# Optimization experiments

Measured on AMD Instinct MI355X. Metric: run time of the kernel, lower is better.

## Reference

```python
import math
import jax, jax.numpy as jnp
import numpy as np

N_EMBED = 1024
N_HEAD = 16
B, T = 2, 2048


def _gelu_tanh(x):
    # GPT-2 tanh-approx GELU
    c = math.sqrt(2.0 / math.pi)
    return 0.5 * x * (1.0 + jnp.tanh(c * (x + 0.044715 * x * x * x)))


def _layer_norm(x, w, b, eps=1e-5):
    mu = jnp.mean(x, axis=-1, keepdims=True)
    var = jnp.var(x, axis=-1, keepdims=True)
    return (x - mu) * jax.lax.rsqrt(var + eps) * w + b


def setup_inputs() -> dict:
    key = jax.random.key(0)
    ks = jax.random.split(key, 8)
    s = lambda fan_in: 1.0 / math.sqrt(fan_in)
    return {
        "x": jax.random.normal(ks[0], (B, T, N_EMBED), jnp.float32),
        "ln1_w": jnp.ones((N_EMBED,), jnp.float32),
        "ln1_b": jnp.zeros((N_EMBED,), jnp.float32),
        "W_attn": jax.random.normal(ks[1], (N_EMBED, 3 * N_EMBED), jnp.float32) * s(N_EMBED),
        "b_attn": jnp.zeros((3 * N_EMBED,), jnp.float32),
        "W_o": jax.random.normal(ks[2], (N_EMBED, N_EMBED), jnp.float32) * s(N_EMBED),
        "b_o": jnp.zeros((N_EMBED,), jnp.float32),
        "ln2_w": jnp.ones((N_EMBED,), jnp.float32),
        "ln2_b": jnp.zeros((N_EMBED,), jnp.float32),
        "W_fc": jax.random.normal(ks[3], (N_EMBED, 4 * N_EMBED), jnp.float32) * s(N_EMBED),
        "b_fc": jnp.zeros((4 * N_EMBED,), jnp.float32),
        "W_proj": jax.random.normal(ks[4], (4 * N_EMBED, N_EMBED), jnp.float32) * s(4 * N_EMBED),
        "b_proj": jnp.zeros((N_EMBED,), jnp.float32),
    }


def reference(x, ln1_w, ln1_b, W_attn, b_attn, W_o, b_o,
              ln2_w, ln2_b, W_fc, b_fc, W_proj, b_proj):
    Bx, Tx, C = x.shape
    H = N_HEAD
    Dh = C // H

    # --- attention ---
    h = _layer_norm(x, ln1_w, ln1_b)
    qkv = h @ W_attn + b_attn                       # [B,T,3C]
    q, k, v = jnp.split(qkv, 3, axis=-1)
    q = q.reshape(Bx, Tx, H, Dh).transpose(0, 2, 1, 3)   # [B,H,T,Dh]
    k = k.reshape(Bx, Tx, H, Dh).transpose(0, 2, 1, 3)
    v = v.reshape(Bx, Tx, H, Dh).transpose(0, 2, 1, 3)

    attn = jnp.einsum("bhqd,bhkd->bhqk", q, k) * (1.0 / math.sqrt(Dh))
    causal = jnp.tril(jnp.ones((Tx, Tx), dtype=bool))
    attn = jnp.where(causal[None, None], attn, -jnp.inf)
    attn = jax.nn.softmax(attn, axis=-1)
    y = jnp.einsum("bhqk,bhkd->bhqd", attn, v)      # [B,H,T,Dh]
    y = y.transpose(0, 2, 1, 3).reshape(Bx, Tx, C)
    y = y @ W_o + b_o
    x = x + y

    # --- MLP ---
    h = _layer_norm(x, ln2_w, ln2_b)
    h = _gelu_tanh(h @ W_fc + b_fc)
    h = h @ W_proj + b_proj
    return x + h
```

## Files before the change

kernel.cpp:

```cpp
#include <hip/hip_runtime.h>
#include <math.h>

constexpr int TDIM = 2048;
constexpr int BDIM = 2;
constexpr int CDIM = 1024;
constexpr int HEADS = 16;
constexpr int DH = 64;
constexpr int MDIM = BDIM * TDIM;

typedef short bf16x8 __attribute__((ext_vector_type(8)));
typedef float f32x4 __attribute__((ext_vector_type(4)));
typedef float f32x16 __attribute__((ext_vector_type(16)));

__device__ __forceinline__ float b2f(unsigned short u) {
    union { float f; unsigned int i; } v; v.i = ((unsigned int)u) << 16; return v.f;
}
__device__ __forceinline__ unsigned short f2b(float f) {
    union { float f; unsigned int i; } v; v.f = f;
    unsigned int r = (v.i + 0x7FFFu + ((v.i >> 16) & 1u)) >> 16;
    return (unsigned short)r;
}
__device__ __forceinline__ unsigned int cvtpk(float lo, float hi) {
    unsigned int r;
    asm("v_cvt_pk_bf16_f32 %0, %1, %2" : "=v"(r) : "v"(lo), "v"(hi));
    return r;
}
__device__ __forceinline__ float gelu_f(float x) {
    float z = -2.3022077f * (x + 0.044715f * x * x * x);
    return x / (1.0f + exp2f(z));
}
__device__ __forceinline__ void async_copy16(const void* g, void* l) {
    __builtin_amdgcn_global_load_lds(
        (const __attribute__((address_space(1))) unsigned int*)g,
        (__attribute__((address_space(3))) unsigned int*)l, 16, 0, 0);
}

#define PBAR do { asm volatile("" ::: "memory"); __builtin_amdgcn_s_barrier(); \
                  asm volatile("" ::: "memory"); } while (0)
#define LGKM0 asm volatile("s_waitcnt lgkmcnt(0)" ::: "memory")

__global__ __launch_bounds__(256) void transpose_cast(
    const float* __restrict__ W, unsigned short* __restrict__ Wt, int K, int N) {
    __shared__ float tile[32][33];
    int n0 = blockIdx.x * 32, k0 = blockIdx.y * 32;
    int tx = threadIdx.x & 31, ty = threadIdx.x >> 5;
#pragma unroll
    for (int i = 0; i < 32; i += 8)
        tile[ty + i][tx] = W[(size_t)(k0 + ty + i) * N + n0 + tx];
    __syncthreads();
#pragma unroll
    for (int i = 0; i < 32; i += 8)
        Wt[(size_t)(n0 + ty + i) * K + k0 + tx] = f2b(tile[tx][ty + i]);
}

__global__ __launch_bounds__(256) void ln_kernel(
    const float* __restrict__ x, const float* __restrict__ w,
    const float* __restrict__ b, unsigned short* __restrict__ out) {
    int row = blockIdx.x;
    int tid = threadIdx.x;
    const float* xr = x + (size_t)row * CDIM;
    float4 v = *(const float4*)(xr + tid * 4);
    float s  = v.x + v.y + v.z + v.w;
    float ss = v.x * v.x + v.y * v.y + v.z * v.z + v.w * v.w;
#pragma unroll
    for (int off = 32; off >= 1; off >>= 1) {
        s  += __shfl_xor(s, off);
        ss += __shfl_xor(ss, off);
    }
    __shared__ float rs[4], rss[4];
    int wave = tid >> 6;
    if ((tid & 63) == 0) { rs[wave] = s; rss[wave] = ss; }
    __syncthreads();
    s  = rs[0] + rs[1] + rs[2] + rs[3];
    ss = rss[0] + rss[1] + rss[2] + rss[3];
    float mean = s * (1.0f / CDIM);
    float var  = ss * (1.0f / CDIM) - mean * mean;
    float rstd = rsqrtf(var + 1e-5f);
    float4 wv = *(const float4*)(w + tid * 4);
    float4 bv = *(const float4*)(b + tid * 4);
    ushort4 o;
    o.x = f2b((v.x - mean) * rstd * wv.x + bv.x);
    o.y = f2b((v.y - mean) * rstd * wv.y + bv.y);
    o.z = f2b((v.z - mean) * rstd * wv.z + bv.z);
    o.w = f2b((v.w - mean) * rstd * wv.w + bv.w);
    *(ushort4*)(out + (size_t)row * CDIM + tid * 4) = o;
}

template <int MODE>
__global__ __launch_bounds__(512, 2) void gemm256(
    const unsigned short* __restrict__ A, const unsigned short* __restrict__ Wt,
    const float* __restrict__ bias, void* __restrict__ Cout, int M, int N, int K) {
    __shared__ __align__(16) short As[2][256 * 64];
    __shared__ __align__(16) short Bs[2][256 * 64];
    const int tid = threadIdx.x;
    const int lane = tid & 63, w = tid >> 6;
    const int wm = w >> 2, wn = w & 3;
    const int h = lane >> 4, r15 = lane & 15;
    const int sr = lane >> 3;
    const int sc = 8 * ((lane & 7) ^ sr);

    const int nwg = gridDim.x * gridDim.y;
    const int bid = blockIdx.y * gridDim.x + blockIdx.x;
    const int nbid = (bid & 7) * (nwg >> 3) + (bid >> 3);
    const int bx = nbid % gridDim.x;
    const int by = nbid / gridDim.x;
    const int row0 = by * 256, col0 = bx * 256;

    const unsigned short* gA = A  + (size_t)(row0 + w * 8 + sr) * K + sc;
    const unsigned short* gB = Wt + (size_t)(col0 + w * 8 + sr) * K + sc;

    f32x4 acc[8][4] = {};
    bf16x8 aA[4][2], bB[4][2];

    auto stA = [&](int kt, int hh) {
        short* dst = &As[kt & 1][(hh * 128 + w * 8) * 64];
        const unsigned short* src = gA + (size_t)(hh * 128) * K + (size_t)kt * 64;
        async_copy16(src, dst);
        async_copy16(src + (size_t)64 * K, dst + 64 * 64);
    };
    auto stB = [&](int kt, int hh) {
        short* dst = &Bs[kt & 1][(hh * 128 + w * 8) * 64];
        const unsigned short* src = gB + (size_t)(hh * 128) * K + (size_t)kt * 64;
        async_copy16(src, dst);
        async_copy16(src + (size_t)64 * K, dst + 64 * 64);
    };
    auto rdA = [&](const short* S, int rh) {
#pragma unroll
        for (int ii = 0; ii < 4; ++ii)
#pragma unroll
            for (int ks = 0; ks < 2; ++ks) {
                int ra = wm * 128 + rh * 64 + ii * 16 + r15;
                int off = ra * 128 + ((ks * 64 + h * 16) ^ ((ra & 7) << 4));
                aA[ii][ks] = *(const bf16x8*)((const char*)S + off);
            }
    };
    auto rdB = [&](const short* S, int J0) {
#pragma unroll
        for (int dj = 0; dj < 2; ++dj)
#pragma unroll
            for (int ks = 0; ks < 2; ++ks) {
                int rb = wn * 64 + (J0 + dj) * 16 + r15;
                int off = rb * 128 + ((ks * 64 + h * 16) ^ ((rb & 7) << 4));
                bB[J0 + dj][ks] = *(const bf16x8*)((const char*)S + off);
            }
    };
    auto mm = [&](int rh, int ch) {
        __builtin_amdgcn_s_setprio(1);
#pragma unroll
        for (int ii = 0; ii < 4; ++ii)
#pragma unroll
            for (int jj = 0; jj < 2; ++jj)
#pragma unroll
                for (int ks = 0; ks < 2; ++ks)
                    acc[rh * 4 + ii][ch * 2 + jj] = __builtin_amdgcn_mfma_f32_16x16x32_bf16(
                        aA[ii][ks], bB[ch * 2 + jj][ks], acc[rh * 4 + ii][ch * 2 + jj], 0, 0, 0);
        __builtin_amdgcn_s_setprio(0);
    };

    const int niter = K >> 7;

    stA(0, 0); stB(0, 0); stB(0, 1); stA(0, 1);
    stA(1, 0); stB(1, 0); stB(1, 1);
    asm volatile("s_waitcnt vmcnt(6)" ::: "memory");
    PBAR;

    for (int t = 0; t < niter; ++t) {
        const bool st = (t + 1 < niter);
        const int t2 = 2 * t + 2, t3 = 2 * t + 3;
        rdA(As[0], 0); rdB(Bs[0], 0);
        stA(2 * t + 1, 1);
        PBAR; LGKM0; mm(0, 0); PBAR;
        rdB(Bs[0], 2);
        PBAR; LGKM0; mm(0, 1); PBAR;
        rdA(As[0], 1);
        if (st) stB(t2, 0);
        PBAR; LGKM0; mm(1, 0); PBAR;
        if (st) {
            stB(t2, 1);
            stA(t2, 0);
            asm volatile("s_waitcnt vmcnt(6)" ::: "memory");
        } else {
            asm volatile("s_waitcnt vmcnt(0)" ::: "memory");
        }
        PBAR; LGKM0; mm(1, 1); PBAR;
        rdA(As[1], 0); rdB(Bs[1], 0);
        if (st) stA(t2, 1);
        PBAR; LGKM0; mm(0, 0); PBAR;
        rdB(Bs[1], 2);
        PBAR; LGKM0; mm(0, 1); PBAR;
        rdA(As[1], 1);
        if (st) stB(t3, 0);
        PBAR; LGKM0; mm(1, 0); PBAR;
        if (st) {
            stB(t3, 1);
            stA(t3, 0);
            asm volatile("s_waitcnt vmcnt(6)" ::: "memory");
        } else {
            asm volatile("s_waitcnt vmcnt(0)" ::: "memory");
        }
        PBAR; LGKM0; mm(1, 1); PBAR;
    }

#pragma unroll
    for (int I = 0; I < 8; ++I) {
#pragma unroll
        for (int J = 0; J < 4; ++J) {
            int cc = col0 + wn * 64 + J * 16 + r15;
            float bv = bias[cc];
#pragma unroll
            for (int q = 0; q < 4; ++q) {
                int rr = row0 + wm * 128 + I * 16 + h * 4 + q;
                float v = acc[I][J][q] + bv;
                if (MODE == 2) v = gelu_f(v);
                ((unsigned short*)Cout)[(size_t)rr * N + cc] = f2b(v);
            }
        }
    }
}

template <int MODE, int BN, int NBUF>
__global__ __launch_bounds__(256) void gemm_bf16(
    const unsigned short* __restrict__ A, const unsigned short* __restrict__ Wt,
    const float* __restrict__ bias, const float* __restrict__ res,
    void* __restrict__ Cout, int M, int N, int K) {
    constexpr int JF = BN / 32;
    constexpr int INF = 4 + JF;
    __shared__ __align__(16) short As[NBUF][128 * 64];
    __shared__ __align__(16) short Bs[NBUF][BN * 64];
    const int tid = threadIdx.x;
    const int lane = tid & 63, w = tid >> 6;
    const int wr = w >> 1, wc = w & 1;

    const int nwg = gridDim.x * gridDim.y;
    const int bid = blockIdx.y * gridDim.x + blockIdx.x;
    const int nbid = (bid & 7) * (nwg >> 3) + (bid >> 3);
    const int bx = nbid % gridDim.x;
    const int by = nbid / gridDim.x;
    const int row0 = by * 128, col0 = bx * BN;

    const int sr = lane >> 3;
    const int sc = 8 * ((lane & 7) ^ sr);
    const unsigned short* gA = A  + (size_t)(row0 + w * 8 + sr) * K + sc;
    const unsigned short* gB = Wt + (size_t)(col0 + w * 8 + sr) * K + sc;

    f32x4 acc[4][JF] = {};
    const int h = lane >> 4;
    const int r15 = lane & 15;
    const int nt = K >> 6;

#pragma unroll
    for (int pt = 0; pt < NBUF - 1; ++pt) {
        const int kp = pt << 6;
#pragma unroll
        for (int i = 0; i < 4; ++i)
            async_copy16(gA + (size_t)i * 32 * K + kp, &As[pt][(w * 8 + i * 32) * 64]);
#pragma unroll
        for (int i = 0; i < JF; ++i)
            async_copy16(gB + (size_t)i * 32 * K + kp, &Bs[pt][(w * 8 + i * 32) * 64]);
    }

    for (int t = 0; t < nt; ++t) {
        const int cur = t % NBUF;
        const int tp = t + NBUF - 1;
        if (tp < nt) {
            const int bufp = tp % NBUF;
            const int kp = tp << 6;
#pragma unroll
            for (int i = 0; i < 4; ++i)
                async_copy16(gA + (size_t)i * 32 * K + kp, &As[bufp][(w * 8 + i * 32) * 64]);
#pragma unroll
            for (int i = 0; i < JF; ++i)
                async_copy16(gB + (size_t)i * 32 * K + kp, &Bs[bufp][(w * 8 + i * 32) * 64]);
            asm volatile("s_waitcnt vmcnt(%0)" :: "n"((NBUF - 1) * INF) : "memory");
        } else {
            asm volatile("s_waitcnt vmcnt(0)" ::: "memory");
        }
        __builtin_amdgcn_s_barrier();
        asm volatile("" ::: "memory");

#pragma unroll
        for (int ks = 0; ks < 2; ++ks) {
            bf16x8 af[4], bfr[JF];
#pragma unroll
            for (int i = 0; i < 4; ++i) {
                int ra = wr * 64 + i * 16 + r15;
                int offa = ra * 128 + ((ks * 64 + h * 16) ^ ((ra & 7) << 4));
                af[i] = *(const bf16x8*)((const char*)As[cur] + offa);
            }
#pragma unroll
            for (int j = 0; j < JF; ++j) {
                int rb = wc * (BN / 2) + j * 16 + r15;
                int offb = rb * 128 + ((ks * 64 + h * 16) ^ ((rb & 7) << 4));
                bfr[j] = *(const bf16x8*)((const char*)Bs[cur] + offb);
            }
#pragma unroll
            for (int i = 0; i < 4; ++i)
#pragma unroll
                for (int j = 0; j < JF; ++j)
                    acc[i][j] = __builtin_amdgcn_mfma_f32_16x16x32_bf16(
                        af[i], bfr[j], acc[i][j], 0, 0, 0);
        }
        asm volatile("" ::: "memory");
        __builtin_amdgcn_s_barrier();
    }

#pragma unroll
    for (int i = 0; i < 4; ++i) {
#pragma unroll
        for (int j = 0; j < JF; ++j) {
            int c = col0 + wc * (BN / 2) + j * 16 + r15;
            float bv = bias[c];
#pragma unroll
            for (int q = 0; q < 4; ++q) {
                int rr = row0 + wr * 64 + i * 16 + h * 4 + q;
                float v = acc[i][j][q] + bv;
                if (MODE == 2) v = gelu_f(v);
                if (MODE == 1) v += res[(size_t)rr * N + c];
                if (MODE == 1) ((float*)Cout)[(size_t)rr * N + c] = v;
                else ((unsigned short*)Cout)[(size_t)rr * N + c] = f2b(v);
            }
        }
    }
}

__global__ __launch_bounds__(512, 4) void attn_mfma(
    const unsigned short* __restrict__ qkv, unsigned short* __restrict__ y) {
    const int bh = blockIdx.x;
    const int b = bh >> 4, hh = bh & 15;
    const int by = blockIdx.y;
    const int qy = (by < 8) ? (15 - by) : (by - 8);
    const int q0 = qy * 128;
    const int tid = threadIdx.x;
    const int lane = tid & 63, w = tid >> 6;
    const int p = w & 3, half = w >> 2;
    const int hi = lane >> 5, q31 = lane & 31;

    const float SC  = 0.1803368801111244f;
    const float THR = 44.0f;

    __shared__ __align__(16) char smem[36864];
    float (*Os)[68] = (float (*)[68])smem;
    float* mlm = (float*)(smem + 34816);
    float* mll = (float*)(smem + 34816 + 1024);

    const size_t base = (size_t)b * TDIM * (3 * CDIM);
    const unsigned short* qb = qkv + base + hh * DH;
    const unsigned short* kb = qkv + base + CDIM + hh * DH;
    const unsigned short* vb = qkv + base + 2 * CDIM + hh * DH;

    const int gq = q0 + p * 32 + q31;
    const int qmin_w = q0 + p * 32;
    const int qmax_w = qmin_w + 31;

    bf16x8 qf[4];
#pragma unroll
    for (int ks = 0; ks < 4; ++ks)
        qf[ks] = *(const bf16x8*)(qb + (size_t)gq * (3 * CDIM) + ks * 16 + hi * 8);

    const int sr = lane >> 3;
    const int scK = 8 * ((lane & 7) ^ sr);
    const int rV = tid >> 3;
    const int dblk = (tid & 7) * 8;

    f32x16 oacc[2] = {};
    float m = -1e30f, l = 0.f;
    bf16x8 vreg;

    const int NT = 2 * qy + 2;

    {
        short* Ks0 = (short*)smem;
        int rowbase = w * 8;
        async_copy16(kb + (size_t)(rowbase + sr) * (3 * CDIM) + scK, Ks0 + rowbase * 64);
        vreg = *(const bf16x8*)(vb + (size_t)rV * (3 * CDIM) + dblk);
        char* Vt0 = smem + 16384;
#pragma unroll
        for (int j = 0; j < 8; ++j) {
            int d = dblk + j;
            int swz = ((d ^ (d >> 3)) & 7) << 4;
            *(short*)(Vt0 + d * 128 + ((2 * rV) ^ swz)) = vreg[j];
        }
    }
    __syncthreads();

    for (int kt = 0; kt < NT; ++kt) {
        const int c = kt & 1;
        const char* Ksc = smem + c * 8192;
        const char* Vtc = smem + 16384 + c * 8192;
        const bool pre = (kt + 1 < NT);

        if (pre) {
            const int kv1 = (kt + 1) * 64;
            short* Ksn = (short*)(smem + (c ^ 1) * 8192);
            int rowbase = w * 8;
            async_copy16(kb + (size_t)(kv1 + rowbase + sr) * (3 * CDIM) + scK,
                         Ksn + rowbase * 64);
            vreg = *(const bf16x8*)(vb + (size_t)(kv1 + rV) * (3 * CDIM) + dblk);
        }

        const int kvs = kt * 64 + half * 32;
        if (kvs <= qmax_w) {
            f32x16 sacc = {};
            __builtin_amdgcn_s_setprio(1);
#pragma unroll
            for (int ks = 0; ks < 4; ++ks) {
                int row = half * 32 + q31;
                int off = row * 128 + ((32 * ks + 16 * hi) ^ ((row & 7) << 4));
                bf16x8 kf = *(const bf16x8*)(Ksc + off);
                sacc = __builtin_amdgcn_mfma_f32_32x32x16_bf16(kf, qf[ks], sacc, 0, 0, 0);
            }
            __builtin_amdgcn_s_setprio(0);

            float p_[16];
            if (kvs + 31 > qmin_w) {
#pragma unroll
                for (int r = 0; r < 16; ++r) {
                    int kvg = kvs + (r & 3) + 8 * (r >> 2) + 4 * hi;
                    p_[r] = (kvg > gq) ? -1e30f : sacc[r];
                }
            } else {
#pragma unroll
                for (int r = 0; r < 16; ++r) p_[r] = sacc[r];
            }

            float t8[8];
#pragma unroll
            for (int r = 0; r < 8; ++r) t8[r] = fmaxf(p_[r], p_[r + 8]);
#pragma unroll
            for (int r = 0; r < 4; ++r) t8[r] = fmaxf(t8[r], t8[r + 4]);
            float pm = fmaxf(fmaxf(t8[0], t8[1]), fmaxf(t8[2], t8[3]));
            pm = fmaxf(pm, __shfl_xor(pm, 32));

            if (!__all(pm <= m + THR)) {
                float mnew = fmaxf(m, pm);
                float sf = exp2f((m - mnew) * SC);
                m = mnew;
                l *= sf;
                oacc[0] *= sf;
                oacc[1] *= sf;
            }
            float mc = m * SC;
#pragma unroll
            for (int r = 0; r < 16; ++r) p_[r] = exp2f(fmaf(p_[r], SC, -mc));
#pragma unroll
            for (int r = 0; r < 8; ++r) t8[r] = p_[r] + p_[r + 8];
#pragma unroll
            for (int r = 0; r < 4; ++r) t8[r] = t8[r] + t8[r + 4];
            float rsum = (t8[0] + t8[1]) + (t8[2] + t8[3]);
            rsum += __shfl_xor(rsum, 32);
            l += rsum;

            bf16x8 pa[2];
#pragma unroll
            for (int k2 = 0; k2 < 2; ++k2) {
                unsigned int A0 = cvtpk(p_[8 * k2 + 0], p_[8 * k2 + 1]);
                unsigned int A1 = cvtpk(p_[8 * k2 + 2], p_[8 * k2 + 3]);
                unsigned int B0 = cvtpk(p_[8 * k2 + 4], p_[8 * k2 + 5]);
                unsigned int B1 = cvtpk(p_[8 * k2 + 6], p_[8 * k2 + 7]);
                unsigned int sA0 = __shfl_xor((int)A0, 32);
                unsigned int sA1 = __shfl_xor((int)A1, 32);
                unsigned int sB0 = __shfl_xor((int)B0, 32);
                unsigned int sB1 = __shfl_xor((int)B1, 32);
                union { int i[4]; bf16x8 h; } u;
                u.i[0] = hi ? (int)sB0 : (int)A0;
                u.i[1] = hi ? (int)sB1 : (int)A1;
                u.i[2] = hi ? (int)B0 : (int)sA0;
                u.i[3] = hi ? (int)B1 : (int)sA1;
                pa[k2] = u.h;
            }

            __builtin_amdgcn_s_setprio(1);
#pragma unroll
            for (int j2 = 0; j2 < 2; ++j2) {
                int row = 32 * j2 + q31;
                int swz = ((row ^ (row >> 3)) & 7) << 4;
#pragma unroll
                for (int k2 = 0; k2 < 2; ++k2) {
                    int off = row * 128 + ((64 * half + 32 * k2 + 16 * hi) ^ swz);
                    bf16x8 vf = *(const bf16x8*)(Vtc + off);
                    oacc[j2] = __builtin_amdgcn_mfma_f32_32x32x16_bf16(vf, pa[k2], oacc[j2], 0, 0, 0);
                }
            }
            __builtin_amdgcn_s_setprio(0);
        }

        if (pre) {
            char* Vtn = smem + 16384 + (c ^ 1) * 8192;
#pragma unroll
            for (int j = 0; j < 8; ++j) {
                int d = dblk + j;
                int swz = ((d ^ (d >> 3)) & 7) << 4;
                *(short*)(Vtn + d * 128 + ((2 * rV) ^ swz)) = vreg[j];
            }
        }
        __syncthreads();
    }

    mlm[(half * 4 + p) * 32 + q31] = m;
    mll[(half * 4 + p) * 32 + q31] = l;
    __syncthreads();
    float mo = mlm[((half ^ 1) * 4 + p) * 32 + q31];
    float lo = mll[((half ^ 1) * 4 + p) * 32 + q31];
    float M  = fmaxf(m, mo);
    float sf  = exp2f((m - M) * SC);
    float sfo = exp2f((mo - M) * SC);
    float invl = 1.0f / (l * sf + lo * sfo);

    if (half == 1) {
#pragma unroll
        for (int j2 = 0; j2 < 2; ++j2)
#pragma unroll
            for (int g = 0; g < 4; ++g) {
                float4 v4 = make_float4(oacc[j2][4 * g + 0] * sf, oacc[j2][4 * g + 1] * sf,
                                        oacc[j2][4 * g + 2] * sf, oacc[j2][4 * g + 3] * sf);
                *(float4*)&Os[p * 32 + q31][32 * j2 + 8 * g + 4 * hi] = v4;
            }
    }
    __syncthreads();
    if (half == 0) {
#pragma unroll
        for (int j2 = 0; j2 < 2; ++j2)
#pragma unroll
            for (int g = 0; g < 4; ++g) {
                float4 t = *(const float4*)&Os[p * 32 + q31][32 * j2 + 8 * g + 4 * hi];
                float4 v4;
                v4.x = (oacc[j2][4 * g + 0] * sf + t.x) * invl;
                v4.y = (oacc[j2][4 * g + 1] * sf + t.y) * invl;
                v4.z = (oacc[j2][4 * g + 2] * sf + t.z) * invl;
                v4.w = (oacc[j2][4 * g + 3] * sf + t.w) * invl;
                *(float4*)&Os[p * 32 + q31][32 * j2 + 8 * g + 4 * hi] = v4;
            }
    }
    __syncthreads();

    const int r0 = tid >> 4;
    const int c4 = (tid & 15) * 4;
#pragma unroll
    for (int pass = 0; pass < 4; ++pass) {
        int row = pass * 32 + r0;
        float4 v = *(const float4*)&Os[row][c4];
        ushort4 o;
        o.x = f2b(v.x); o.y = f2b(v.y); o.z = f2b(v.z); o.w = f2b(v.w);
        *(ushort4*)(y + (size_t)(b * TDIM + q0 + row) * CDIM + hh * DH + c4) = o;
    }
}

extern "C" void kernel_launch(void* const* d_in, const int* in_sizes, int n_in,
                              void* d_out, int out_size, void* d_ws, size_t ws_size,
                              hipStream_t stream) {
    const float* x      = (const float*)d_in[0];
    const float* ln1_w  = (const float*)d_in[1];
    const float* ln1_b  = (const float*)d_in[2];
    const float* W_attn = (const float*)d_in[3];
    const float* b_attn = (const float*)d_in[4];
    const float* W_o    = (const float*)d_in[5];
    const float* b_o    = (const float*)d_in[6];
    const float* ln2_w  = (const float*)d_in[7];
    const float* ln2_b  = (const float*)d_in[8];
    const float* W_fc   = (const float*)d_in[9];
    const float* b_fc   = (const float*)d_in[10];
    const float* W_proj = (const float*)d_in[11];
    const float* b_proj = (const float*)d_in[12];
    float* out = (float*)d_out;

    char* ws = (char*)d_ws;
    const size_t MB = 1024 * 1024;
    unsigned short* h_bf    = (unsigned short*)(ws);
    unsigned short* big     = (unsigned short*)(ws + 8 * MB);
    unsigned short* Wt_attn = (unsigned short*)(ws + 40 * MB);
    unsigned short* Wt_o    = (unsigned short*)(ws + 46 * MB);
    unsigned short* Wt_fc   = (unsigned short*)(ws + 48 * MB);
    unsigned short* Wt_proj = (unsigned short*)(ws + 56 * MB);
    float* x1 = out;

    hipLaunchKernelGGL(transpose_cast, dim3(96, 32),  dim3(256), 0, stream, W_attn, Wt_attn, CDIM, 3 * CDIM);
    hipLaunchKernelGGL(transpose_cast, dim3(32, 32),  dim3(256), 0, stream, W_o,    Wt_o,    CDIM, CDIM);
    hipLaunchKernelGGL(transpose_cast, dim3(128, 32), dim3(256), 0, stream, W_fc,   Wt_fc,   CDIM, 4 * CDIM);
    hipLaunchKernelGGL(transpose_cast, dim3(32, 128), dim3(256), 0, stream, W_proj, Wt_proj, 4 * CDIM, CDIM);

    hipLaunchKernelGGL(ln_kernel, dim3(MDIM), dim3(256), 0, stream, x, ln1_w, ln1_b, h_bf);
    hipLaunchKernelGGL((gemm256<0>), dim3(3 * CDIM / 256, MDIM / 256), dim3(512), 0,
                       stream, h_bf, Wt_attn, b_attn, big, MDIM, 3 * CDIM, CDIM);
    hipLaunchKernelGGL(attn_mfma, dim3(BDIM * HEADS, TDIM / 128), dim3(512), 0, stream,
                       big, h_bf);
    hipLaunchKernelGGL((gemm_bf16<1, 64, 3>), dim3(CDIM / 64, MDIM / 128), dim3(256), 0,
                       stream, h_bf, Wt_o, b_o, x, x1, MDIM, CDIM, CDIM);
    hipLaunchKernelGGL(ln_kernel, dim3(MDIM), dim3(256), 0, stream, x1, ln2_w, ln2_b, h_bf);
    hipLaunchKernelGGL((gemm256<2>), dim3(4 * CDIM / 256, MDIM / 256), dim3(512), 0,
                       stream, h_bf, Wt_fc, b_fc, big, MDIM, 4 * CDIM, CDIM);
    hipLaunchKernelGGL((gemm_bf16<1, 64, 3>), dim3(CDIM / 64, MDIM / 128), dim3(256), 0,
                       stream, big, Wt_proj, b_proj, x1, out, MDIM, CDIM, 4 * CDIM);
}
```

Baseline: 236.1 us.

## Split-K the MLP projection GEMM using the 256x256 kernel plus a reduction

The down-projection GEMM (K=4096) moves from the 128x64-tile kernel to the larger 256x256 gemm256 kernel. K is split four ways across blockIdx.z, giving 256 workgroups. Each split writes bf16 partial sums to a workspace buffer, and a new reduce4 kernel adds the partials, bias and residual into the fp32 output. This trades better MFMA tile efficiency and occupancy for an extra kernel launch, roughly 48MB of additional partial-buffer traffic, and an extra bf16 rounding of the partials. The workspace is relaid out so the partial buffer can reuse the regions holding the attention and FC weights and h_bf, which are no longer needed by this point.

After: 233.1 us (median of 2 runs). Within noise of the previous version (-1.3%).

```diff
diff --git a/kernel.cpp b/kernel.cpp
--- a/kernel.cpp
+++ b/kernel.cpp
@@ -89,7 +89,8 @@
 template <int MODE>
 __global__ __launch_bounds__(512, 2) void gemm256(
     const unsigned short* __restrict__ A, const unsigned short* __restrict__ Wt,
-    const float* __restrict__ bias, void* __restrict__ Cout, int M, int N, int K) {
+    const float* __restrict__ bias, void* __restrict__ Cout, int M, int N,
+    int Kfull, int Klen) {
     __shared__ __align__(16) short As[2][256 * 64];
     __shared__ __align__(16) short Bs[2][256 * 64];
     const int tid = threadIdx.x;
@@ -98,6 +99,7 @@
     const int h = lane >> 4, r15 = lane & 15;
     const int sr = lane >> 3;
     const int sc = 8 * ((lane & 7) ^ sr);
+    const int k0 = (MODE == 3) ? (int)blockIdx.z * Klen : 0;
 
     const int nwg = gridDim.x * gridDim.y;
     const int bid = blockIdx.y * gridDim.x + blockIdx.x;
@@ -106,23 +108,23 @@
     const int by = nbid / gridDim.x;
     const int row0 = by * 256, col0 = bx * 256;
 
-    const unsigned short* gA = A  + (size_t)(row0 + w * 8 + sr) * K + sc;
-    const unsigned short* gB = Wt + (size_t)(col0 + w * 8 + sr) * K + sc;
+    const unsigned short* gA = A  + (size_t)(row0 + w * 8 + sr) * Kfull + k0 + sc;
+    const unsigned short* gB = Wt + (size_t)(col0 + w * 8 + sr) * Kfull + k0 + sc;
 
     f32x4 acc[8][4] = {};
     bf16x8 aA[4][2], bB[4][2];
 
     auto stA = [&](int kt, int hh) {
         short* dst = &As[kt & 1][(hh * 128 + w * 8) * 64];
-        const unsigned short* src = gA + (size_t)(hh * 128) * K + (size_t)kt * 64;
+        const unsigned short* src = gA + (size_t)(hh * 128) * Kfull + (size_t)kt * 64;
         async_copy16(src, dst);
-        async_copy16(src + (size_t)64 * K, dst + 64 * 64);
+        async_copy16(src + (size_t)64 * Kfull, dst + 64 * 64);
     };
     auto stB = [&](int kt, int hh) {
         short* dst = &Bs[kt & 1][(hh * 128 + w * 8) * 64];
-        const unsigned short* src = gB + (size_t)(hh * 128) * K + (size_t)kt * 64;
+        const unsigned short* src = gB + (size_t)(hh * 128) * Kfull + (size_t)kt * 64;
         async_copy16(src, dst);
-        async_copy16(src + (size_t)64 * K, dst + 64 * 64);
+        async_copy16(src + (size_t)64 * Kfull, dst + 64 * 64);
     };
     auto rdA = [&](const short* S, int rh) {
 #pragma unroll
@@ -157,7 +159,7 @@
         __builtin_amdgcn_s_setprio(0);
     };
 
-    const int niter = K >> 7;
+    const int niter = Klen >> 7;
 
     stA(0, 0); stB(0, 0); stB(0, 1); stA(0, 1);
     stA(1, 0); stB(1, 0); stB(1, 1);
@@ -201,21 +203,42 @@
         PBAR; LGKM0; mm(1, 1); PBAR;
     }
 
+    unsigned short* Cp = (unsigned short*)Cout;
+    if (MODE == 3) Cp += (size_t)blockIdx.z * M * N;
 #pragma unroll
     for (int I = 0; I < 8; ++I) {
 #pragma unroll
         for (int J = 0; J < 4; ++J) {
             int cc = col0 + wn * 64 + J * 16 + r15;
-            float bv = bias[cc];
+            float bv = (MODE == 3) ? 0.0f : bias[cc];
 #pragma unroll
             for (int q = 0; q < 4; ++q) {
                 int rr = row0 + wm * 128 + I * 16 + h * 4 + q;
                 float v = acc[I][J][q] + bv;
                 if (MODE == 2) v = gelu_f(v);
-                ((unsigned short*)Cout)[(size_t)rr * N + cc] = f2b(v);
-            }
-        }
-    }
+                Cp[(size_t)rr * N + cc] = f2b(v);
+            }
+        }
+    }
+}
+
+__global__ __launch_bounds__(256) void reduce4(
+    const unsigned short* __restrict__ P, const float* __restrict__ bias,
+    const float* __restrict__ res, float* __restrict__ out) {
+    const size_t eb = ((size_t)blockIdx.x * 256 + threadIdx.x) * 4;
+    const int n = (int)(eb & (CDIM - 1));
+    float4 a = make_float4(0.f, 0.f, 0.f, 0.f);
+    const size_t stride = (size_t)MDIM * CDIM;
+#pragma unroll
+    for (int s = 0; s < 4; ++s) {
+        ushort4 p = *(const ushort4*)(P + s * stride + eb);
+        a.x += b2f(p.x); a.y += b2f(p.y); a.z += b2f(p.z); a.w += b2f(p.w);
+    }
+    float4 bv = *(const float4*)(bias + n);
+    float4 rv = *(const float4*)(res + eb);
+    a.x += bv.x + rv.x; a.y += bv.y + rv.y;
+    a.z += bv.z + rv.z; a.w += bv.w + rv.w;
+    *(float4*)(out + eb) = a;
 }
 
 template <int MODE, int BN, int NBUF>
@@ -565,12 +588,13 @@
 
     char* ws = (char*)d_ws;
     const size_t MB = 1024 * 1024;
-    unsigned short* h_bf    = (unsigned short*)(ws);
-    unsigned short* big     = (unsigned short*)(ws + 8 * MB);
+    unsigned short* big     = (unsigned short*)(ws);
+    unsigned short* Wt_proj = (unsigned short*)(ws + 32 * MB);
     unsigned short* Wt_attn = (unsigned short*)(ws + 40 * MB);
     unsigned short* Wt_o    = (unsigned short*)(ws + 46 * MB);
     unsigned short* Wt_fc   = (unsigned short*)(ws + 48 * MB);
-    unsigned short* Wt_proj = (unsigned short*)(ws + 56 * MB);
+    unsigned short* h_bf    = (unsigned short*)(ws + 56 * MB);
+    unsigned short* Ppart   = (unsigned short*)(ws + 40 * MB);
     float* x1 = out;
 
     hipLaunchKernelGGL(transpose_cast, dim3(96, 32),  dim3(256), 0, stream, W_attn, Wt_attn, CDIM, 3 * CDIM);
@@ -579,15 +603,17 @@
     hipLaunchKernelGGL(transpose_cast, dim3(32, 128), dim3(256), 0, stream, W_proj, Wt_proj, 4 * CDIM, CDIM);
 
     hipLaunchKernelGGL(ln_kernel, dim3(MDIM), dim3(256), 0, stream, x, ln1_w, ln1_b, h_bf);
-    hipLaunchKernelGGL((gemm256<0>), dim3(3 * CDIM / 256, MDIM / 256), dim3(512), 0,
-                       stream, h_bf, Wt_attn, b_attn, big, MDIM, 3 * CDIM, CDIM);
+    hipLaunchKernelGGL((gemm256<0>), dim3(3 * CDIM / 256, MDIM / 256, 1), dim3(512), 0,
+                       stream, h_bf, Wt_attn, b_attn, big, MDIM, 3 * CDIM, CDIM, CDIM);
     hipLaunchKernelGGL(attn_mfma, dim3(BDIM * HEADS, TDIM / 128), dim3(512), 0, stream,
                        big, h_bf);
     hipLaunchKernelGGL((gemm_bf16<1, 64, 3>), dim3(CDIM / 64, MDIM / 128), dim3(256), 0,
                        stream, h_bf, Wt_o, b_o, x, x1, MDIM, CDIM, CDIM);
     hipLaunchKernelGGL(ln_kernel, dim3(MDIM), dim3(256), 0, stream, x1, ln2_w, ln2_b, h_bf);
-    hipLaunchKernelGGL((gemm256<2>), dim3(4 * CDIM / 256, MDIM / 256), dim3(512), 0,
-                       stream, h_bf, Wt_fc, b_fc, big, MDIM, 4 * CDIM, CDIM);
-    hipLaunchKernelGGL((gemm_bf16<1, 64, 3>), dim3(CDIM / 64, MDIM / 128), dim3(256), 0,
-                       stream, big, Wt_proj, b_proj, x1, out, MDIM, CDIM, 4 * CDIM);
-}
+    hipLaunchKernelGGL((gemm256<2>), dim3(4 * CDIM / 256, MDIM / 256, 1), dim3(512), 0,
+                       stream, h_bf, Wt_fc, b_fc, big, MDIM, 4 * CDIM, CDIM, CDIM);
+    hipLaunchKernelGGL((gemm256<3>), dim3(CDIM / 256, MDIM / 256, 4), dim3(512), 0,
+                       stream, big, Wt_proj, b_proj, Ppart, MDIM, CDIM, 4 * CDIM, CDIM);
+    hipLaunchKernelGGL(reduce4, dim3(MDIM * CDIM / 4 / 256), dim3(256), 0, stream,
+                       Ppart, b_proj, x1, out);
+}
```
